# Performance work log

Measured on AMD Instinct MI355X. Metric: run time of the kernel, lower is better.

The kernel has to match this reference:

```python
import jax, jax.numpy as jnp
import numpy as np

D_MODEL = 1024
NUM_HEADS = 16
DEPTH = D_MODEL // NUM_HEADS
MAX_LEN = 5000


def _make_pe(d_model=D_MODEL, max_len=MAX_LEN):
    # Faithful to torch PositionalEncoding: pe shape [max_len, 1, d_model]
    position = np.arange(max_len, dtype=np.float32)[:, None]
    div_term = np.exp(np.arange(0, d_model, 2, dtype=np.float32) * (-np.log(10000.0) / d_model))
    pe = np.zeros((max_len, d_model), dtype=np.float32)
    pe[:, 0::2] = np.sin(position * div_term)
    pe[:, 1::2] = np.cos(position * div_term)
    return jnp.asarray(pe[:, None, :])  # [max_len, 1, d_model]


def setup_inputs() -> dict:
    key = jax.random.key(0)
    ks = jax.random.split(key, 11)
    B, S, D = 4, 2048, D_MODEL
    s = 1.0 / np.sqrt(D)
    inp = {
        "v": jax.random.normal(ks[0], (B, S, D), jnp.float32),
        "k": jax.random.normal(ks[1], (B, S, D), jnp.float32),
        "q": jax.random.normal(ks[2], (B, S, D), jnp.float32),
        "wq_w": jax.random.normal(ks[3], (D, D), jnp.float32) * s,
        "wq_b": jnp.zeros((D,), jnp.float32),
        "wk_w": jax.random.normal(ks[4], (D, D), jnp.float32) * s,
        "wk_b": jnp.zeros((D,), jnp.float32),
        "wv_w": jax.random.normal(ks[5], (D, D), jnp.float32) * s,
        "wv_b": jnp.zeros((D,), jnp.float32),
        "dense_w": jax.random.normal(ks[6], (D, D), jnp.float32) * s,
        "dense_b": jnp.zeros((D,), jnp.float32),
        "pe": _make_pe(),
    }
    return inp


def _split_heads(x, B):
    # [B, S, D] -> [B, H, S, depth]
    return x.reshape(B, -1, NUM_HEADS, DEPTH).transpose(0, 2, 1, 3)


def reference(v, k, q, wq_w, wq_b, wk_w, wk_b, wv_w, wv_b, dense_w, dense_b, pe):
    B = q.shape[0]
    # Faithful bug-reproduction: pe[:batch] has shape [B, 1, D], broadcast over seq.
    pe_b = pe[:B]  # [B, 1, D]
    q = q + pe_b
    k = k + pe_b
    v = v + pe_b
    # Linear layers (torch: x @ W.T + b)
    qh = _split_heads(q @ wq_w.T + wq_b, B)  # [B,H,Sq,d]
    kh = _split_heads(k @ wk_w.T + wk_b, B)  # [B,H,Sk,d]
    vh = _split_heads(v @ wv_w.T + wv_b, B)  # [B,H,Sk,d]
    scale = 1.0 / jnp.sqrt(jnp.float32(DEPTH))
    logits = jnp.einsum("bhqd,bhkd->bhqk", qh, kh) * scale
    attn = jax.nn.softmax(logits, axis=-1)
    out = jnp.einsum("bhqk,bhkd->bhqd", attn, vh)
    out = out.transpose(0, 2, 1, 3).reshape(B, -1, D_MODEL)
    return out @ dense_w.T + dense_b
```

## Files before the change

### kernel.cpp

```cpp
#include <hip/hip_runtime.h>
#include <hip/hip_bf16.h>

typedef short short8 __attribute__((ext_vector_type(8)));
typedef float f32x4 __attribute__((ext_vector_type(4)));
typedef float f32x16 __attribute__((ext_vector_type(16)));
typedef unsigned int uint4v __attribute__((ext_vector_type(4)));

#define MFMA16(a, b, c) __builtin_amdgcn_mfma_f32_16x16x32_bf16(a, b, c, 0, 0, 0)
#define MFMA32(a, b, c) __builtin_amdgcn_mfma_f32_32x32x16_bf16(a, b, c, 0, 0, 0)

typedef __attribute__((address_space(1))) const unsigned int gas_u32;
typedef __attribute__((address_space(3))) unsigned int las_u32;

__device__ inline void gll16(const void* g, void* l) {
    __builtin_amdgcn_global_load_lds((gas_u32*)g, (las_u32*)l, 16, 0, 0);
}

__device__ inline unsigned short f2bf(float f) {
    unsigned u = __builtin_bit_cast(unsigned, f);
    u += 0x7fff + ((u >> 16) & 1);
    return (unsigned short)(u >> 16);
}

__device__ inline unsigned pk_trunc(float a, float b) {
    unsigned ua = __builtin_bit_cast(unsigned, a);
    unsigned ub = __builtin_bit_cast(unsigned, b);
    return (ua >> 16) | (ub & 0xFFFF0000u);
}

__device__ inline float exp2_fast(float x) {
#if __has_builtin(__builtin_amdgcn_exp2f)
    return __builtin_amdgcn_exp2f(x);
#else
    float r; asm("v_exp_f32 %0, %1" : "=v"(r) : "v"(x)); return r;
#endif
}

__device__ inline void pl32_swap(unsigned &a, unsigned &b) {
    asm volatile("v_permlane32_swap_b32 %0, %1" : "+v"(a), "+v"(b));
}

__global__ void pe_cast3(const float* __restrict__ q, const float* __restrict__ k,
                         const float* __restrict__ v, const float* __restrict__ pe,
                         unsigned short* __restrict__ oq, unsigned short* __restrict__ ok,
                         unsigned short* __restrict__ ov) {
    const float* x = (blockIdx.y == 0) ? q : (blockIdx.y == 1) ? k : v;
    unsigned short* o = (blockIdx.y == 0) ? oq : (blockIdx.y == 1) ? ok : ov;
    int i = blockIdx.x * 256 + threadIdx.x;
    long e = (long)i * 4;
    int b = (int)(e >> 21);
    int d = (int)(e & 1023);
    float4 xv = reinterpret_cast<const float4*>(x)[i];
    float4 pv = *reinterpret_cast<const float4*>(pe + b * 1024 + d);
    ushort4 r;
    r.x = f2bf(xv.x + pv.x); r.y = f2bf(xv.y + pv.y);
    r.z = f2bf(xv.z + pv.z); r.w = f2bf(xv.w + pv.w);
    reinterpret_cast<ushort4*>(o)[i] = r;
}

__global__ void wcast4(const float* __restrict__ w0, const float* __restrict__ w1,
                       const float* __restrict__ w2, const float* __restrict__ w3,
                       unsigned short* __restrict__ o0) {
    const float* w = (blockIdx.y == 0) ? w0 : (blockIdx.y == 1) ? w1
                   : (blockIdx.y == 2) ? w2 : w3;
    unsigned short* o = o0 + (size_t)blockIdx.y * 1024 * 1024;
    int i = blockIdx.x * 256 + threadIdx.x;
    float4 xv = reinterpret_cast<const float4*>(w)[i];
    ushort4 r;
    r.x = f2bf(xv.x); r.y = f2bf(xv.y); r.z = f2bf(xv.z); r.w = f2bf(xv.w);
    reinterpret_cast<ushort4*>(o)[i] = r;
}

__global__ __launch_bounds__(256) void gemm_qkv(const unsigned short* __restrict__ X0,
                                                const unsigned short* __restrict__ W0,
                                                const float* __restrict__ bq,
                                                const float* __restrict__ bk,
                                                const float* __restrict__ bv,
                                                unsigned short* __restrict__ oq,
                                                unsigned short* __restrict__ ok,
                                                unsigned short* __restrict__ ov,
                                                float qscale) {
    const int K = 1024;
    int z = blockIdx.z;
    const unsigned short* A = X0 + (size_t)z * 8192 * 1024;
    const unsigned short* W = W0 + (size_t)z * 1024 * 1024;
    const float* bias = (z == 0) ? bq : (z == 1) ? bk : bv;
    unsigned short* out = (z == 0) ? oq : (z == 1) ? ok : ov;
    float scale = (z == 0) ? qscale : 1.0f;

    __shared__ unsigned short lsA[128 * 32];
    __shared__ unsigned short lsB[128 * 32];
    int tid = threadIdx.x;
    int wave = tid >> 6, lane = tid & 63, lg = lane >> 4, l15 = lane & 15;
    int brow = blockIdx.x * 128;
    int bcol = blockIdx.y * 128;
    int wr = wave >> 1, wc = wave & 1;

    f32x4 zero4 = {0.f, 0.f, 0.f, 0.f};
    f32x4 acc[4][4];
#pragma unroll
    for (int m = 0; m < 4; ++m)
#pragma unroll
        for (int n = 0; n < 4; ++n) acc[m][n] = zero4;

    for (int k0 = 0; k0 < K; k0 += 32) {
#pragma unroll
        for (int j = 0; j < 2; ++j) {
            int c = j * 256 + wave * 64 + lane;
            const unsigned short* srcA = A + ((long)(brow + (c >> 2)) * K + k0 + (c & 3) * 8);
            const unsigned short* srcB = W + ((long)(bcol + (c >> 2)) * K + k0 + (c & 3) * 8);
            char* dstA = (char*)lsA + (j * 256 + wave * 64) * 16;
            char* dstB = (char*)lsB + (j * 256 + wave * 64) * 16;
            gll16(srcA, dstA);
            gll16(srcB, dstB);
        }
        __syncthreads();
        short8 af[4], bf_[4];
#pragma unroll
        for (int m = 0; m < 4; ++m) {
            int row = wr * 64 + m * 16 + l15;
            af[m] = *(const short8*)((const char*)lsA + row * 64 + lg * 16);
        }
#pragma unroll
        for (int n = 0; n < 4; ++n) {
            int col = wc * 64 + n * 16 + l15;
            bf_[n] = *(const short8*)((const char*)lsB + col * 64 + lg * 16);
        }
#pragma unroll
        for (int m = 0; m < 4; ++m)
#pragma unroll
            for (int n = 0; n < 4; ++n) acc[m][n] = MFMA16(af[m], bf_[n], acc[m][n]);
        __syncthreads();
    }

#pragma unroll
    for (int m = 0; m < 4; ++m)
#pragma unroll
        for (int n = 0; n < 4; ++n) {
            int col = bcol + wc * 64 + n * 16 + l15;
            float bv_ = bias[col];
#pragma unroll
            for (int r = 0; r < 4; ++r) {
                int row = brow + wr * 64 + m * 16 + lg * 4 + r;
                float v = (acc[m][n][r] + bv_) * scale;
                int b = row >> 11, s = row & 2047;
                if (z < 2) {
                    int h = col >> 6, d = col & 63;
                    out[(((long)(b * 16 + h) * 2048 + s) * 64 + d)] = f2bf(v);
                } else {
                    out[((long)(b * 1024 + col)) * 2048 + s] = f2bf(v);
                }
            }
        }
}

__global__ __launch_bounds__(256) void gemm_dense(const unsigned short* __restrict__ A,
                                                  const unsigned short* __restrict__ W,
                                                  const float* __restrict__ bias,
                                                  float* __restrict__ out) {
    const int K = 1024;
    __shared__ unsigned short lsA[128 * 32];
    __shared__ unsigned short lsB[128 * 32];
    int tid = threadIdx.x;
    int wave = tid >> 6, lane = tid & 63, lg = lane >> 4, l15 = lane & 15;
    int brow = blockIdx.x * 128;
    int bcol = blockIdx.y * 128;
    int wr = wave >> 1, wc = wave & 1;

    f32x4 zero4 = {0.f, 0.f, 0.f, 0.f};
    f32x4 acc[4][4];
#pragma unroll
    for (int m = 0; m < 4; ++m)
#pragma unroll
        for (int n = 0; n < 4; ++n) acc[m][n] = zero4;

    for (int k0 = 0; k0 < K; k0 += 32) {
#pragma unroll
        for (int j = 0; j < 2; ++j) {
            int c = j * 256 + wave * 64 + lane;
            const unsigned short* srcA = A + ((long)(brow + (c >> 2)) * K + k0 + (c & 3) * 8);
            const unsigned short* srcB = W + ((long)(bcol + (c >> 2)) * K + k0 + (c & 3) * 8);
            char* dstA = (char*)lsA + (j * 256 + wave * 64) * 16;
            char* dstB = (char*)lsB + (j * 256 + wave * 64) * 16;
            gll16(srcA, dstA);
            gll16(srcB, dstB);
        }
        __syncthreads();
        short8 af[4], bf_[4];
#pragma unroll
        for (int m = 0; m < 4; ++m) {
            int row = wr * 64 + m * 16 + l15;
            af[m] = *(const short8*)((const char*)lsA + row * 64 + lg * 16);
        }
#pragma unroll
        for (int n = 0; n < 4; ++n) {
            int col = wc * 64 + n * 16 + l15;
            bf_[n] = *(const short8*)((const char*)lsB + col * 64 + lg * 16);
        }
#pragma unroll
        for (int m = 0; m < 4; ++m)
#pragma unroll
            for (int n = 0; n < 4; ++n) acc[m][n] = MFMA16(af[m], bf_[n], acc[m][n]);
        __syncthreads();
    }

#pragma unroll
    for (int m = 0; m < 4; ++m)
#pragma unroll
        for (int n = 0; n < 4; ++n) {
            int col = bcol + wc * 64 + n * 16 + l15;
            float bv = bias[col];
#pragma unroll
            for (int r = 0; r < 4; ++r) {
                int row = brow + wr * 64 + m * 16 + lg * 4 + r;
                out[(long)row * 1024 + col] = acc[m][n][r] + bv;
            }
        }
}

__global__ __launch_bounds__(256) void attn_kernel(const unsigned short* __restrict__ Qh,
                                                   const unsigned short* __restrict__ Kh,
                                                   const unsigned short* __restrict__ Vt,
                                                   unsigned short* __restrict__ Om) {
    const int S = 2048;
    const int NT = S / 64;
    int flat = blockIdx.x;
    int nf_ = (flat & 7) * 128 + (flat >> 3);
    int qt = nf_ & 15;
    int bh = nf_ >> 4;
    int b = bh >> 4, h = bh & 15;

    int tid = threadIdx.x, wave = tid >> 6, lane = tid & 63;
    int l31 = lane & 31, hi = lane >> 5;

    __shared__ __align__(16) unsigned short Kl[3][4096];
    __shared__ __align__(16) unsigned short Vtl[3][4096];

    const unsigned short* Qb = Qh + (long)bh * S * 64;
    const unsigned short* Kb = Kh + (long)bh * S * 64;
    const unsigned short* Vb = Vt + (long)bh * 64 * S;

    int colS = ((((tid & 7) * 16) ^ (((tid >> 3) & 7) << 4)) >> 1);
    const unsigned short* srcK = Kb + (tid >> 3) * 64 + colS;
    const unsigned short* srcV = Vb + (tid >> 3) * 2048 + colS;

    short8 aq[4];
    {
        const unsigned short* qrow = Qb + (long)(qt * 128 + wave * 32 + l31) * 64 + hi * 8;
#pragma unroll
        for (int s = 0; s < 4; ++s) aq[s] = *(const short8*)(qrow + s * 16);
    }

    f32x16 oacc[2], lacc;
#pragma unroll
    for (int r = 0; r < 16; ++r) { oacc[0][r] = 0.f; oacc[1][r] = 0.f; lacc[r] = 0.f; }

    const short8 ones8 = {0x3F80, 0x3F80, 0x3F80, 0x3F80, 0x3F80, 0x3F80, 0x3F80, 0x3F80};

    int rb0 = l31 * 128;
    int swz = (l31 & 7) << 4;

#define STAGE(kt, bi) do {                                              \
        const unsigned short* sk = srcK + (kt) * 4096;                  \
        gll16(sk,         (char*)Kl[bi] + wave * 1024);                 \
        gll16(sk + 2048,  (char*)Kl[bi] + 4096 + wave * 1024);          \
        const unsigned short* sv = srcV + (kt) * 64;                    \
        gll16(sv,         (char*)Vtl[bi] + wave * 1024);                \
        gll16(sv + 65536, (char*)Vtl[bi] + 4096 + wave * 1024);         \
    } while (0)

    STAGE(0, 0);
    STAGE(1, 1);

    int bi = 0, sb = 2;
    for (int kt = 0; kt < NT; ++kt) {
        if (kt == NT - 1) { asm volatile("s_waitcnt vmcnt(0)" ::: "memory"); }
        else              { asm volatile("s_waitcnt vmcnt(4)" ::: "memory"); }
        __builtin_amdgcn_s_barrier();
        if (kt < NT - 2) STAGE(kt + 2, sb);

        const char* KlC = (const char*)Kl[bi];
        const char* VlC = (const char*)Vtl[bi];

        f32x16 sacc[2];
#pragma unroll
        for (int r = 0; r < 16; ++r) { sacc[0][r] = 0.f; sacc[1][r] = 0.f; }
#pragma unroll
        for (int blk = 0; blk < 2; ++blk)
#pragma unroll
            for (int s = 0; s < 4; ++s) {
                short8 kf = *(const short8*)(KlC + blk * 4096 + rb0 + ((32 * s + 16 * hi) ^ swz));
                sacc[blk] = MFMA32(kf, aq[s], sacc[blk]);
            }

#pragma unroll
        for (int blk = 0; blk < 2; ++blk)
#pragma unroll
            for (int r = 0; r < 16; ++r) sacc[blk][r] = exp2_fast(sacc[blk][r]);

#pragma unroll
        for (int s = 0; s < 4; ++s) {
            const int blk = s >> 1, base = (s & 1) * 8;
            unsigned q0 = pk_trunc(sacc[blk][base + 0], sacc[blk][base + 1]);
            unsigned q1 = pk_trunc(sacc[blk][base + 2], sacc[blk][base + 3]);
            unsigned q2 = pk_trunc(sacc[blk][base + 4], sacc[blk][base + 5]);
            unsigned q3 = pk_trunc(sacc[blk][base + 6], sacc[blk][base + 7]);
            pl32_swap(q0, q2);
            pl32_swap(q1, q3);
            uint4v pw; pw[0] = q0; pw[1] = q1; pw[2] = q2; pw[3] = q3;
            short8 pa = __builtin_bit_cast(short8, pw);
#pragma unroll
            for (int dblk = 0; dblk < 2; ++dblk) {
                short8 vf = *(const short8*)(VlC + dblk * 4096 + rb0 + ((32 * s + 16 * hi) ^ swz));
                oacc[dblk] = MFMA32(pa, vf, oacc[dblk]);
            }
            lacc = MFMA32(pa, ones8, lacc);
        }
        bi = (bi == 2) ? 0 : bi + 1;
        sb = (sb == 2) ? 0 : sb + 1;
    }
#undef STAGE

    float inv[16];
#pragma unroll
    for (int r = 0; r < 16; ++r) inv[r] = 1.0f / lacc[r];

    int qrow0 = qt * 128 + wave * 32 + 4 * hi;
#pragma unroll
    for (int dblk = 0; dblk < 2; ++dblk)
#pragma unroll
        for (int r = 0; r < 16; ++r) {
            int qrow = qrow0 + (r & 3) + 8 * (r >> 2);
            int d = h * 64 + dblk * 32 + l31;
            float v = oacc[dblk][r] * inv[r];
            Om[((long)b * 2048 + qrow) * 1024 + d] = f2bf(v);
        }
}

extern "C" void kernel_launch(void* const* d_in, const int* in_sizes, int n_in,
                              void* d_out, int out_size, void* d_ws, size_t ws_size,
                              hipStream_t stream) {
    const float* v_in = (const float*)d_in[0];
    const float* k_in = (const float*)d_in[1];
    const float* q_in = (const float*)d_in[2];
    const float* wq_w = (const float*)d_in[3];
    const float* wq_b = (const float*)d_in[4];
    const float* wk_w = (const float*)d_in[5];
    const float* wk_b = (const float*)d_in[6];
    const float* wv_w = (const float*)d_in[7];
    const float* wv_b = (const float*)d_in[8];
    const float* wd_w = (const float*)d_in[9];
    const float* wd_b = (const float*)d_in[10];
    const float* pe   = (const float*)d_in[11];

    const long SZ = 8192L * 1024 * 2;
    char* ws = (char*)d_ws;
    unsigned short* xq = (unsigned short*)(ws + 0);
    unsigned short* xk = (unsigned short*)(ws + SZ);
    unsigned short* xv = (unsigned short*)(ws + 2 * SZ);
    unsigned short* qh = (unsigned short*)(ws + 3 * SZ);
    unsigned short* kh = (unsigned short*)(ws + 4 * SZ);
    unsigned short* vt = (unsigned short*)(ws + 5 * SZ);
    unsigned short* wqb16 = (unsigned short*)(ws + 6 * SZ);

    pe_cast3<<<dim3(8192, 3), 256, 0, stream>>>(q_in, k_in, v_in, pe, xq, xk, xv);
    wcast4<<<dim3(1024, 4), 256, 0, stream>>>(wq_w, wk_w, wv_w, wd_w, wqb16);

    const float QSCALE = 0.125f * 1.44269504088896f;
    gemm_qkv<<<dim3(64, 8, 3), 256, 0, stream>>>(xq, wqb16, wq_b, wk_b, wv_b,
                                                 qh, kh, vt, QSCALE);
    unsigned short* om = xq;
    attn_kernel<<<1024, 256, 0, stream>>>(qh, kh, vt, om);
    gemm_dense<<<dim3(64, 8), 256, 0, stream>>>(om, wqb16 + 3L * 1024 * 1024, wd_b,
                                                (float*)d_out);
}
```

Before: 233.9 us.

## Process two 32-row Q fragments per wave in attention to reuse K/V tiles

Each wave now handles 64 query rows (two 32-row fragments) instead of 32, so every block covers 256 queries and the grid halves to 512 blocks. Each K and V fragment read from LDS feeds two MFMAs, and the K/V global loads per query are halved. The cost is doubled accumulator registers (launch bounds set to 2 blocks per CU) and fewer blocks, which lowers occupancy and parallelism on a 256-CU device.

After: 219.6 us. -6.1%, faster.

```diff
diff --git a/kernel.cpp b/kernel.cpp
--- a/kernel.cpp
+++ b/kernel.cpp
@@ -218,16 +218,16 @@
         }
 }
 
-__global__ __launch_bounds__(256) void attn_kernel(const unsigned short* __restrict__ Qh,
-                                                   const unsigned short* __restrict__ Kh,
-                                                   const unsigned short* __restrict__ Vt,
-                                                   unsigned short* __restrict__ Om) {
+__global__ __launch_bounds__(256, 2) void attn_kernel(const unsigned short* __restrict__ Qh,
+                                                      const unsigned short* __restrict__ Kh,
+                                                      const unsigned short* __restrict__ Vt,
+                                                      unsigned short* __restrict__ Om) {
     const int S = 2048;
     const int NT = S / 64;
     int flat = blockIdx.x;
-    int nf_ = (flat & 7) * 128 + (flat >> 3);
-    int qt = nf_ & 15;
-    int bh = nf_ >> 4;
+    int nf_ = (flat & 7) * 64 + (flat >> 3);
+    int qt = nf_ & 7;
+    int bh = nf_ >> 3;
     int b = bh >> 4, h = bh & 15;
 
     int tid = threadIdx.x, wave = tid >> 6, lane = tid & 63;
@@ -244,16 +244,23 @@
     const unsigned short* srcK = Kb + (tid >> 3) * 64 + colS;
     const unsigned short* srcV = Vb + (tid >> 3) * 2048 + colS;
 
-    short8 aq[4];
+    short8 aq[2][4];
     {
-        const unsigned short* qrow = Qb + (long)(qt * 128 + wave * 32 + l31) * 64 + hi * 8;
-#pragma unroll
-        for (int s = 0; s < 4; ++s) aq[s] = *(const short8*)(qrow + s * 16);
-    }
-
-    f32x16 oacc[2], lacc;
-#pragma unroll
-    for (int r = 0; r < 16; ++r) { oacc[0][r] = 0.f; oacc[1][r] = 0.f; lacc[r] = 0.f; }
+        const unsigned short* qrow = Qb + (long)(qt * 256 + wave * 64 + l31) * 64 + hi * 8;
+#pragma unroll
+        for (int qf = 0; qf < 2; ++qf)
+#pragma unroll
+            for (int s = 0; s < 4; ++s)
+                aq[qf][s] = *(const short8*)(qrow + qf * 32 * 64 + s * 16);
+    }
+
+    f32x16 oacc[2][2], lacc[2];
+#pragma unroll
+    for (int r = 0; r < 16; ++r) {
+        oacc[0][0][r] = 0.f; oacc[0][1][r] = 0.f;
+        oacc[1][0][r] = 0.f; oacc[1][1][r] = 0.f;
+        lacc[0][r] = 0.f; lacc[1][r] = 0.f;
+    }
 
     const short8 ones8 = {0x3F80, 0x3F80, 0x3F80, 0x3F80, 0x3F80, 0x3F80, 0x3F80, 0x3F80};
 
@@ -282,59 +289,73 @@
         const char* KlC = (const char*)Kl[bi];
         const char* VlC = (const char*)Vtl[bi];
 
-        f32x16 sacc[2];
-#pragma unroll
-        for (int r = 0; r < 16; ++r) { sacc[0][r] = 0.f; sacc[1][r] = 0.f; }
+        f32x16 sacc[2][2];
+#pragma unroll
+        for (int r = 0; r < 16; ++r) {
+            sacc[0][0][r] = 0.f; sacc[0][1][r] = 0.f;
+            sacc[1][0][r] = 0.f; sacc[1][1][r] = 0.f;
+        }
 #pragma unroll
         for (int blk = 0; blk < 2; ++blk)
 #pragma unroll
             for (int s = 0; s < 4; ++s) {
                 short8 kf = *(const short8*)(KlC + blk * 4096 + rb0 + ((32 * s + 16 * hi) ^ swz));
-                sacc[blk] = MFMA32(kf, aq[s], sacc[blk]);
-            }
-
-#pragma unroll
-        for (int blk = 0; blk < 2; ++blk)
-#pragma unroll
-            for (int r = 0; r < 16; ++r) sacc[blk][r] = exp2_fast(sacc[blk][r]);
+                sacc[0][blk] = MFMA32(kf, aq[0][s], sacc[0][blk]);
+                sacc[1][blk] = MFMA32(kf, aq[1][s], sacc[1][blk]);
+            }
+
+#pragma unroll
+        for (int qf = 0; qf < 2; ++qf)
+#pragma unroll
+            for (int blk = 0; blk < 2; ++blk)
+#pragma unroll
+                for (int r = 0; r < 16; ++r) sacc[qf][blk][r] = exp2_fast(sacc[qf][blk][r]);
 
 #pragma unroll
         for (int s = 0; s < 4; ++s) {
             const int blk = s >> 1, base = (s & 1) * 8;
-            unsigned q0 = pk_trunc(sacc[blk][base + 0], sacc[blk][base + 1]);
-            unsigned q1 = pk_trunc(sacc[blk][base + 2], sacc[blk][base + 3]);
-            unsigned q2 = pk_trunc(sacc[blk][base + 4], sacc[blk][base + 5]);
-            unsigned q3 = pk_trunc(sacc[blk][base + 6], sacc[blk][base + 7]);
-            pl32_swap(q0, q2);
-            pl32_swap(q1, q3);
-            uint4v pw; pw[0] = q0; pw[1] = q1; pw[2] = q2; pw[3] = q3;
-            short8 pa = __builtin_bit_cast(short8, pw);
+            short8 pa[2];
+#pragma unroll
+            for (int qf = 0; qf < 2; ++qf) {
+                unsigned q0 = pk_trunc(sacc[qf][blk][base + 0], sacc[qf][blk][base + 1]);
+                unsigned q1 = pk_trunc(sacc[qf][blk][base + 2], sacc[qf][blk][base + 3]);
+                unsigned q2 = pk_trunc(sacc[qf][blk][base + 4], sacc[qf][blk][base + 5]);
+                unsigned q3 = pk_trunc(sacc[qf][blk][base + 6], sacc[qf][blk][base + 7]);
+                pl32_swap(q0, q2);
+                pl32_swap(q1, q3);
+                uint4v pw; pw[0] = q0; pw[1] = q1; pw[2] = q2; pw[3] = q3;
+                pa[qf] = __builtin_bit_cast(short8, pw);
+            }
 #pragma unroll
             for (int dblk = 0; dblk < 2; ++dblk) {
                 short8 vf = *(const short8*)(VlC + dblk * 4096 + rb0 + ((32 * s + 16 * hi) ^ swz));
-                oacc[dblk] = MFMA32(pa, vf, oacc[dblk]);
-            }
-            lacc = MFMA32(pa, ones8, lacc);
+                oacc[0][dblk] = MFMA32(pa[0], vf, oacc[0][dblk]);
+                oacc[1][dblk] = MFMA32(pa[1], vf, oacc[1][dblk]);
+            }
+            lacc[0] = MFMA32(pa[0], ones8, lacc[0]);
+            lacc[1] = MFMA32(pa[1], ones8, lacc[1]);
         }
         bi = (bi == 2) ? 0 : bi + 1;
         sb = (sb == 2) ? 0 : sb + 1;
     }
 #undef STAGE
 
-    float inv[16];
-#pragma unroll
-    for (int r = 0; r < 16; ++r) inv[r] = 1.0f / lacc[r];
-
-    int qrow0 = qt * 128 + wave * 32 + 4 * hi;
-#pragma unroll
-    for (int dblk = 0; dblk < 2; ++dblk)
-#pragma unroll
-        for (int r = 0; r < 16; ++r) {
-            int qrow = qrow0 + (r & 3) + 8 * (r >> 2);
-            int d = h * 64 + dblk * 32 + l31;
-            float v = oacc[dblk][r] * inv[r];
-            Om[((long)b * 2048 + qrow) * 1024 + d] = f2bf(v);
-        }
+#pragma unroll
+    for (int qf = 0; qf < 2; ++qf) {
+        float inv[16];
+#pragma unroll
+        for (int r = 0; r < 16; ++r) inv[r] = 1.0f / lacc[qf][r];
+        int qrow0 = qt * 256 + wave * 64 + qf * 32 + 4 * hi;
+#pragma unroll
+        for (int dblk = 0; dblk < 2; ++dblk)
+#pragma unroll
+            for (int r = 0; r < 16; ++r) {
+                int qrow = qrow0 + (r & 3) + 8 * (r >> 2);
+                int d = h * 64 + dblk * 32 + l31;
+                float v = oacc[qf][dblk][r] * inv[r];
+                Om[((long)b * 2048 + qrow) * 1024 + d] = f2bf(v);
+            }
+    }
 }
 
 extern "C" void kernel_launch(void* const* d_in, const int* in_sizes, int n_in,
@@ -370,7 +391,7 @@
     gemm_qkv<<<dim3(64, 8, 3), 256, 0, stream>>>(xq, wqb16, wq_b, wk_b, wv_b,
                                                  qh, kh, vt, QSCALE);
     unsigned short* om = xq;
-    attn_kernel<<<1024, 256, 0, stream>>>(qh, kh, vt, om);
+    attn_kernel<<<512, 256, 0, stream>>>(qh, kh, vt, om);
     gemm_dense<<<dim3(64, 8), 256, 0, stream>>>(om, wqb16 + 3L * 1024 * 1024, wd_b,
                                                 (float*)d_out);
 }
```
